# Kernel tuning notes

Hardware: AMD Instinct MI355X
Metric: run time of the kernel (lower is better)

The kernel has to match this reference:

```python
import jax, jax.numpy as jnp
import numpy as np

B, H, S, DK = 2, 16, 2048, 64


def setup_inputs() -> dict:
    key = jax.random.key(0)
    kq, kk, kv = jax.random.split(key, 3)
    query = jax.random.normal(kq, (B, H, S, DK), dtype=jnp.float32)
    k = jax.random.normal(kk, (B, H, S, DK), dtype=jnp.float32)
    value = jax.random.normal(kv, (B, H, S, DK), dtype=jnp.float32)
    # causal padding-style mask: 1 = keep, 0 = masked (set to -inf pre-softmax)
    mask = jnp.tril(jnp.ones((S, S), dtype=jnp.int32))[None, None, :, :]
    return {"query": query, "key": k, "value": value, "d_k": DK, "mask": mask}


def reference(query, key, value, d_k, mask):
    # scores: [B, H, Sq, Sk]
    scores = jnp.einsum("bhqd,bhkd->bhqk", query, key)
    scores = scores / jnp.sqrt(jnp.asarray(d_k, dtype=scores.dtype))
    scores = jnp.where(mask == 0, -jnp.inf, scores)
    att = jax.nn.softmax(scores, axis=-1)
    # dropout is identity in eval mode (deterministic reference)
    out = jnp.einsum("bhqk,bhkd->bhqd", att, value)
    return out
```

## Files before the change

kernel.cpp:

```cpp
#include <hip/hip_runtime.h>
#include <cstdint>

#define B_ 2
#define H_ 16
#define S_ 2048
#define DK_ 64
#define BH_ (B_*H_)
#define NQT 32
#define BN 128

typedef __attribute__((ext_vector_type(8))) short short8;
typedef __attribute__((ext_vector_type(4))) float floatx4;

__device__ inline unsigned short f2bf(float f) {
  union { float f; unsigned u; } v; v.f = f;
  unsigned u = v.u;
  unsigned r = u + 0x7fffu + ((u >> 16) & 1u);
  return (unsigned short)(r >> 16);
}

__global__ __launch_bounds__(256) void conv_kv(const float* __restrict__ K,
                                               const float* __restrict__ V,
                                               unsigned short* __restrict__ Kb,
                                               unsigned short* __restrict__ Vb) {
  __shared__ __align__(16) unsigned short t[64 * 80];
  const int bh = blockIdx.y, s0 = blockIdx.x * 64;
  const int row = threadIdx.x >> 2, cp = threadIdx.x & 3;

  {
    const float* src = K + ((size_t)(bh * S_ + s0 + row)) * DK_ + cp * 16;
    unsigned short* dst = Kb + ((size_t)(bh * S_ + s0 + row)) * DK_ + cp * 16;
    #pragma unroll
    for (int h = 0; h < 2; ++h) {
      float4 a = *(const float4*)(src + h * 8);
      float4 b = *(const float4*)(src + h * 8 + 4);
      uint4 st;
      st.x = (unsigned)f2bf(a.x) | ((unsigned)f2bf(a.y) << 16);
      st.y = (unsigned)f2bf(a.z) | ((unsigned)f2bf(a.w) << 16);
      st.z = (unsigned)f2bf(b.x) | ((unsigned)f2bf(b.y) << 16);
      st.w = (unsigned)f2bf(b.z) | ((unsigned)f2bf(b.w) << 16);
      *(uint4*)(dst + h * 8) = st;
    }
  }
  {
    const float* src = V + ((size_t)(bh * S_ + s0 + row)) * DK_ + cp * 16;
    #pragma unroll
    for (int j4 = 0; j4 < 4; ++j4) {
      float4 a = *(const float4*)(src + j4 * 4);
      int c = cp * 16 + j4 * 4;
      t[(c + 0) * 80 + row] = f2bf(a.x);
      t[(c + 1) * 80 + row] = f2bf(a.y);
      t[(c + 2) * 80 + row] = f2bf(a.z);
      t[(c + 3) * 80 + row] = f2bf(a.w);
    }
    __syncthreads();
    unsigned short* dst = Vb + ((size_t)(bh * DK_ + row)) * S_ + s0 + cp * 16;
    *(uint4*)(dst)     = *(const uint4*)&t[row * 80 + cp * 16];
    *(uint4*)(dst + 8) = *(const uint4*)&t[row * 80 + cp * 16 + 8];
  }
}

__global__ __launch_bounds__(256, 2)
void fa_kernel(const float* __restrict__ Q, const unsigned short* __restrict__ Kb,
               const unsigned short* __restrict__ Vb, float* __restrict__ Out) {
  __shared__ __align__(16) unsigned short Kt[2][8192];
  __shared__ __align__(16) unsigned short Vt[2][8192];
  __shared__ __align__(16) unsigned short Pt[8192];

  const int tid  = threadIdx.x;
  const int wave = tid >> 6;
  const int lane = tid & 63;
  const int quad = lane >> 4;
  const int l16  = lane & 15;
  const int bh   = blockIdx.y;
  const int qa   = blockIdx.x;
  const int qb   = NQT - 1 - qa;

  const float SCL = 0.125f * 1.44269504088896340736f;

  short8 aqA[2], aqB[2];
  {
    const float* qgA = Q + ((size_t)bh * S_ + qa * 64 + wave * 16 + l16) * DK_;
    const float* qgB = Q + ((size_t)bh * S_ + qb * 64 + wave * 16 + l16) * DK_;
    #pragma unroll
    for (int ks = 0; ks < 2; ++ks) {
      float4 x = *(const float4*)(qgA + ks * 32 + quad * 8);
      float4 y = *(const float4*)(qgA + ks * 32 + quad * 8 + 4);
      short8 t;
      t[0]=(short)f2bf(x.x*SCL); t[1]=(short)f2bf(x.y*SCL); t[2]=(short)f2bf(x.z*SCL); t[3]=(short)f2bf(x.w*SCL);
      t[4]=(short)f2bf(y.x*SCL); t[5]=(short)f2bf(y.y*SCL); t[6]=(short)f2bf(y.z*SCL); t[7]=(short)f2bf(y.w*SCL);
      aqA[ks] = t;
      x = *(const float4*)(qgB + ks * 32 + quad * 8);
      y = *(const float4*)(qgB + ks * 32 + quad * 8 + 4);
      t[0]=(short)f2bf(x.x*SCL); t[1]=(short)f2bf(x.y*SCL); t[2]=(short)f2bf(x.z*SCL); t[3]=(short)f2bf(x.w*SCL);
      t[4]=(short)f2bf(y.x*SCL); t[5]=(short)f2bf(y.y*SCL); t[6]=(short)f2bf(y.z*SCL); t[7]=(short)f2bf(y.w*SCL);
      aqB[ks] = t;
    }
  }

  floatx4 OA[4], OB[4];
  float lA[4], lB[4];
  #pragma unroll
  for (int nt = 0; nt < 4; ++nt) { OA[nt] = (floatx4){0,0,0,0}; OB[nt] = (floatx4){0,0,0,0}; }
  #pragma unroll
  for (int r = 0; r < 4; ++r) { lA[r] = 0.f; lB[r] = 0.f; }

  auto stage = [&](int buf, int kv) {
    #pragma unroll
    for (int rd = 0; rd < 4; ++rd) {
      int cid = rd * 256 + wave * 64 + lane;
      {
        int row = cid >> 3, p = cid & 7, c = p ^ (row & 7);
        const unsigned short* g = Kb + (((size_t)bh * S_ + kv * BN + row) << 6) + (c << 3);
        __builtin_amdgcn_global_load_lds(
            (const __attribute__((address_space(1))) void*)g,
            (__attribute__((address_space(3))) void*)&Kt[buf][(rd * 4 + wave) * 512], 16, 0, 0);
      }
      {
        int row = cid >> 4, p = cid & 15, c = p ^ (row & 15);
        const unsigned short* g = Vb + (((size_t)bh * DK_ + row) << 11) + kv * BN + (c << 3);
        __builtin_amdgcn_global_load_lds(
            (const __attribute__((address_space(1))) void*)g,
            (__attribute__((address_space(3))) void*)&Vt[buf][(rd * 4 + wave) * 512], 16, 0, 0);
      }
    }
  };

  auto compute = [&](const short8* aq, floatx4* Ot, float* lsum,
                     int qt, int kv, int cur, bool domask) {
    float sc[8][4];
    #pragma unroll
    for (int nt = 0; nt < 8; ++nt) {
      floatx4 acc = (floatx4){0.f, 0.f, 0.f, 0.f};
      #pragma unroll
      for (int ks = 0; ks < 2; ++ks) {
        int row = nt * 16 + l16;
        int p = (ks * 4 + quad) ^ (row & 7);
        const short8 bk = *(const short8*)&Kt[cur][row * 64 + p * 8];
        acc = __builtin_amdgcn_mfma_f32_16x16x32_bf16(aq[ks], bk, acc, 0, 0, 0);
      }
      #pragma unroll
      for (int r = 0; r < 4; ++r) sc[nt][r] = acc[r];
    }
    if (domask) {
      #pragma unroll
      for (int nt = 0; nt < 8; ++nt) {
        int col = kv * BN + nt * 16 + l16;
        #pragma unroll
        for (int r = 0; r < 4; ++r) {
          int rowg = qt * 64 + wave * 16 + quad * 4 + r;
          if (col > rowg) sc[nt][r] = -INFINITY;
        }
      }
    }
    #pragma unroll
    for (int nt = 0; nt < 8; ++nt)
      #pragma unroll
      for (int r = 0; r < 4; ++r) {
        float e = __builtin_amdgcn_exp2f(sc[nt][r]);
        lsum[r] += e;
        sc[nt][r] = e;
      }
    __builtin_amdgcn_s_waitcnt(0xC07F);
    __builtin_amdgcn_wave_barrier();
    #pragma unroll
    for (int nt = 0; nt < 8; ++nt) {
      int c = nt * 2 + (l16 >> 3);
      #pragma unroll
      for (int r = 0; r < 4; ++r) {
        int row16 = quad * 4 + r;
        int p = c ^ row16;
        Pt[wave * 2048 + row16 * 128 + p * 8 + (l16 & 7)] = f2bf(sc[nt][r]);
      }
    }
    __builtin_amdgcn_wave_barrier();
    __builtin_amdgcn_s_waitcnt(0xC07F);
    #pragma unroll
    for (int ks = 0; ks < 4; ++ks) {
      int pr = (ks * 4 + quad) ^ l16;
      const short8 ap = *(const short8*)&Pt[wave * 2048 + l16 * 128 + pr * 8];
      #pragma unroll
      for (int nt = 0; nt < 4; ++nt) {
        int row = nt * 16 + l16;
        int p = (ks * 4 + quad) ^ (row & 15);
        const short8 bv = *(const short8*)&Vt[cur][row * 128 + p * 8];
        Ot[nt] = __builtin_amdgcn_mfma_f32_16x16x32_bf16(ap, bv, Ot[nt], 0, 0, 0);
      }
    }
  };

  stage(0, 0);
  __syncthreads();
  const int nkvB = (qb + 2) >> 1;
  const int nkvA = (qa + 2) >> 1;
  for (int kv = 0; kv < nkvB; ++kv) {
    int cur = kv & 1;
    if (kv + 1 < nkvB) stage(cur ^ 1, kv + 1);
    compute(aqB, OB, lB, qb, kv, cur, kv == nkvB - 1);
    if (kv < nkvA) compute(aqA, OA, lA, qa, kv, cur, kv == nkvA - 1);
    __syncthreads();
  }

  #pragma unroll
  for (int r = 0; r < 4; ++r) {
    lB[r] += __shfl_xor(lB[r], 1); lB[r] += __shfl_xor(lB[r], 2);
    lB[r] += __shfl_xor(lB[r], 4); lB[r] += __shfl_xor(lB[r], 8);
    lA[r] += __shfl_xor(lA[r], 1); lA[r] += __shfl_xor(lA[r], 2);
    lA[r] += __shfl_xor(lA[r], 4); lA[r] += __shfl_xor(lA[r], 8);
  }
  {
    float* Og = Out + ((size_t)bh * S_ + qb * 64 + wave * 16) * DK_;
    #pragma unroll
    for (int r = 0; r < 4; ++r) {
      float inv = 1.0f / lB[r];
      #pragma unroll
      for (int nt = 0; nt < 4; ++nt)
        Og[(quad * 4 + r) * DK_ + nt * 16 + l16] = OB[nt][r] * inv;
    }
    Og = Out + ((size_t)bh * S_ + qa * 64 + wave * 16) * DK_;
    #pragma unroll
    for (int r = 0; r < 4; ++r) {
      float inv = 1.0f / lA[r];
      #pragma unroll
      for (int nt = 0; nt < 4; ++nt)
        Og[(quad * 4 + r) * DK_ + nt * 16 + l16] = OA[nt][r] * inv;
    }
  }
}

extern "C" void kernel_launch(void* const* d_in, const int* in_sizes, int n_in,
                              void* d_out, int out_size, void* d_ws, size_t ws_size,
                              hipStream_t stream) {
  const float* Q = (const float*)d_in[0];
  const float* K = (const float*)d_in[1];
  const float* V = (const float*)d_in[2];
  float* Out = (float*)d_out;
  unsigned short* Kb = (unsigned short*)d_ws;
  unsigned short* Vb = Kb + (size_t)BH_ * S_ * DK_;
  conv_kv<<<dim3(S_ / 64, BH_), 256, 0, stream>>>(K, V, Kb, Vb);
  fa_kernel<<<dim3(NQT / 2, BH_), 256, 0, stream>>>(Q, Kb, Vb, Out);
}
```

Before: 146.7 us.

## Compute transposed S=K·Qᵀ, keep P in registers, split KV across waves

Swaps the score MFMA operands so each lane holds scores along the key dimension, then packs exp values straight to bf16 in registers and feeds them to a 16x16x16 MFMA as the B operand. This removes the per-wave LDS round trip for P. V is stored pre-permuted in the conversion kernel to match the new register layout. Waves are split into a 2x2 grid over query halves and KV halves, and the partial O and row sums are reduced through LDS at the end. The 1D grid is also remapped so that blocks with the same qa are adjacent in launch order. This adds an end-of-kernel reduction and uses round-half-up bf16 packing, which rounds slightly differently from the old round-to-nearest-even.

```diff
diff --git a/kernel.cpp b/kernel.cpp
--- a/kernel.cpp
+++ b/kernel.cpp
@@ -7,9 +7,9 @@
 #define DK_ 64
 #define BH_ (B_*H_)
 #define NQT 32
-#define BN 128
 
 typedef __attribute__((ext_vector_type(8))) short short8;
+typedef __attribute__((ext_vector_type(4))) short short4v;
 typedef __attribute__((ext_vector_type(4))) float floatx4;
 
 __device__ inline unsigned short f2bf(float f) {
@@ -17,6 +17,21 @@
   unsigned u = v.u;
   unsigned r = u + 0x7fffu + ((u >> 16) & 1u);
   return (unsigned short)(r >> 16);
+}
+
+__device__ inline floatx4 mfma16(short4v a, short4v b, floatx4 c) {
+#if __has_builtin(__builtin_amdgcn_mfma_f32_16x16x16bf16_1k)
+  return __builtin_amdgcn_mfma_f32_16x16x16bf16_1k(a, b, c, 0, 0, 0);
+#else
+  asm("v_mfma_f32_16x16x16_bf16 %0, %1, %2, %0" : "+v"(c) : "v"(a), "v"(b));
+  return c;
+#endif
+}
+
+__device__ inline short4v u2s4(unsigned a, unsigned b) {
+  union { unsigned u[2]; short4v s; } v;
+  v.u[0] = a; v.u[1] = b;
+  return v.s;
 }
 
 __global__ __launch_bounds__(256) void conv_kv(const float* __restrict__ K,
@@ -54,9 +69,13 @@
       t[(c + 3) * 80 + row] = f2bf(a.w);
     }
     __syncthreads();
-    unsigned short* dst = Vb + ((size_t)(bh * DK_ + row)) * S_ + s0 + cp * 16;
-    *(uint4*)(dst)     = *(const uint4*)&t[row * 80 + cp * 16];
-    *(uint4*)(dst + 8) = *(const uint4*)&t[row * 80 + cp * 16 + 8];
+    const int base128 = s0 & ~127;
+    const int t2 = 2 * ((s0 >> 6) & 1) + (cp >> 1);
+    const int h  = cp & 1;
+    unsigned short* dst = Vb + ((size_t)(bh * DK_ + row)) * S_ + base128 + t2 * 32 + h * 4;
+    #pragma unroll
+    for (int q = 0; q < 4; ++q)
+      *(uint2*)(dst + q * 8) = *(const uint2*)&t[row * 80 + cp * 16 + q * 4];
   }
 }
 
@@ -65,60 +84,62 @@
                const unsigned short* __restrict__ Vb, float* __restrict__ Out) {
   __shared__ __align__(16) unsigned short Kt[2][8192];
   __shared__ __align__(16) unsigned short Vt[2][8192];
-  __shared__ __align__(16) unsigned short Pt[8192];
 
   const int tid  = threadIdx.x;
   const int wave = tid >> 6;
   const int lane = tid & 63;
   const int quad = lane >> 4;
   const int l16  = lane & 15;
-  const int bh   = blockIdx.y;
-  const int qa   = blockIdx.x;
-  const int qb   = NQT - 1 - qa;
+  const int wq   = wave & 1;
+  const int ws   = wave >> 1;
+
+  const int id = blockIdx.x;
+  const int bh = (id & 7) | (((id >> 3) & 3) << 3);
+  const int qa = id >> 5;
+  const int qb = NQT - 1 - qa;
 
   const float SCL = 0.125f * 1.44269504088896340736f;
 
-  short8 aqA[2], aqB[2];
-  {
-    const float* qgA = Q + ((size_t)bh * S_ + qa * 64 + wave * 16 + l16) * DK_;
-    const float* qgB = Q + ((size_t)bh * S_ + qb * 64 + wave * 16 + l16) * DK_;
-    #pragma unroll
-    for (int ks = 0; ks < 2; ++ks) {
-      float4 x = *(const float4*)(qgA + ks * 32 + quad * 8);
-      float4 y = *(const float4*)(qgA + ks * 32 + quad * 8 + 4);
-      short8 t;
-      t[0]=(short)f2bf(x.x*SCL); t[1]=(short)f2bf(x.y*SCL); t[2]=(short)f2bf(x.z*SCL); t[3]=(short)f2bf(x.w*SCL);
-      t[4]=(short)f2bf(y.x*SCL); t[5]=(short)f2bf(y.y*SCL); t[6]=(short)f2bf(y.z*SCL); t[7]=(short)f2bf(y.w*SCL);
-      aqA[ks] = t;
-      x = *(const float4*)(qgB + ks * 32 + quad * 8);
-      y = *(const float4*)(qgB + ks * 32 + quad * 8 + 4);
-      t[0]=(short)f2bf(x.x*SCL); t[1]=(short)f2bf(x.y*SCL); t[2]=(short)f2bf(x.z*SCL); t[3]=(short)f2bf(x.w*SCL);
-      t[4]=(short)f2bf(y.x*SCL); t[5]=(short)f2bf(y.y*SCL); t[6]=(short)f2bf(y.z*SCL); t[7]=(short)f2bf(y.w*SCL);
-      aqB[ks] = t;
-    }
-  }
-
-  floatx4 OA[4], OB[4];
-  float lA[4], lB[4];
+  short8 qfB[4], qfA[4];
+  auto loadQ = [&](int qt, short8* qf) {
+    #pragma unroll
+    for (int nq = 0; nq < 2; ++nq) {
+      const float* p = Q + ((size_t)bh * S_ + qt * 64 + wq * 32 + nq * 16 + l16) * DK_ + quad * 8;
+      #pragma unroll
+      for (int ks = 0; ks < 2; ++ks) {
+        float4 x = *(const float4*)(p + ks * 32);
+        float4 y = *(const float4*)(p + ks * 32 + 4);
+        short8 t;
+        t[0]=(short)f2bf(x.x*SCL); t[1]=(short)f2bf(x.y*SCL); t[2]=(short)f2bf(x.z*SCL); t[3]=(short)f2bf(x.w*SCL);
+        t[4]=(short)f2bf(y.x*SCL); t[5]=(short)f2bf(y.y*SCL); t[6]=(short)f2bf(y.z*SCL); t[7]=(short)f2bf(y.w*SCL);
+        qf[nq * 2 + ks] = t;
+      }
+    }
+  };
+  loadQ(qb, qfB);
+  loadQ(qa, qfA);
+
+  floatx4 OtB[4][2], OtA[4][2];
+  float lB_[2] = {0.f, 0.f}, lA_[2] = {0.f, 0.f};
   #pragma unroll
-  for (int nt = 0; nt < 4; ++nt) { OA[nt] = (floatx4){0,0,0,0}; OB[nt] = (floatx4){0,0,0,0}; }
-  #pragma unroll
-  for (int r = 0; r < 4; ++r) { lA[r] = 0.f; lB[r] = 0.f; }
+  for (int d = 0; d < 4; ++d)
+    #pragma unroll
+    for (int nq = 0; nq < 2; ++nq) { OtB[d][nq] = (floatx4){0,0,0,0}; OtA[d][nq] = (floatx4){0,0,0,0}; }
 
   auto stage = [&](int buf, int kv) {
     #pragma unroll
     for (int rd = 0; rd < 4; ++rd) {
-      int cid = rd * 256 + wave * 64 + lane;
+      const int cid = rd * 256 + wave * 64 + lane;
       {
         int row = cid >> 3, p = cid & 7, c = p ^ (row & 7);
-        const unsigned short* g = Kb + (((size_t)bh * S_ + kv * BN + row) << 6) + (c << 3);
+        const unsigned short* g = Kb + (((size_t)bh * S_ + kv * 128 + row) << 6) + (c << 3);
         __builtin_amdgcn_global_load_lds(
             (const __attribute__((address_space(1))) void*)g,
             (__attribute__((address_space(3))) void*)&Kt[buf][(rd * 4 + wave) * 512], 16, 0, 0);
       }
       {
         int row = cid >> 4, p = cid & 15, c = p ^ (row & 15);
-        const unsigned short* g = Vb + (((size_t)bh * DK_ + row) << 11) + kv * BN + (c << 3);
+        const unsigned short* g = Vb + (((size_t)bh * DK_ + row) << 11) + kv * 128 + (c << 3);
         __builtin_amdgcn_global_load_lds(
             (const __attribute__((address_space(1))) void*)g,
             (__attribute__((address_space(3))) void*)&Vt[buf][(rd * 4 + wave) * 512], 16, 0, 0);
@@ -126,65 +147,57 @@
     }
   };
 
-  auto compute = [&](const short8* aq, floatx4* Ot, float* lsum,
-                     int qt, int kv, int cur, bool domask) {
-    float sc[8][4];
-    #pragma unroll
-    for (int nt = 0; nt < 8; ++nt) {
-      floatx4 acc = (floatx4){0.f, 0.f, 0.f, 0.f};
+  auto computeT = [&](const short8* qf, floatx4 (*Ot)[2], float* ls,
+                      int qt, int kv, int cur, bool domask) {
+    unsigned pk[4][2][2];
+    #pragma unroll
+    for (int nt = 0; nt < 4; ++nt) {
+      const int row = ws * 64 + nt * 16 + l16;
+      floatx4 s0 = (floatx4){0,0,0,0}, s1 = (floatx4){0,0,0,0};
       #pragma unroll
       for (int ks = 0; ks < 2; ++ks) {
-        int row = nt * 16 + l16;
-        int p = (ks * 4 + quad) ^ (row & 7);
-        const short8 bk = *(const short8*)&Kt[cur][row * 64 + p * 8];
-        acc = __builtin_amdgcn_mfma_f32_16x16x32_bf16(aq[ks], bk, acc, 0, 0, 0);
-      }
-      #pragma unroll
-      for (int r = 0; r < 4; ++r) sc[nt][r] = acc[r];
-    }
-    if (domask) {
-      #pragma unroll
-      for (int nt = 0; nt < 8; ++nt) {
-        int col = kv * BN + nt * 16 + l16;
+        const int p = (ks * 4 + quad) ^ (row & 7);
+        const short8 ak = *(const short8*)&Kt[cur][row * 64 + p * 8];
+        s0 = __builtin_amdgcn_mfma_f32_16x16x32_bf16(ak, qf[ks],     s0, 0, 0, 0);
+        s1 = __builtin_amdgcn_mfma_f32_16x16x32_bf16(ak, qf[2 + ks], s1, 0, 0, 0);
+      }
+      if (domask) {
+        const int sb  = kv * 128 + ws * 64 + nt * 16 + quad * 4;
+        const int q0r = qt * 64 + wq * 32 + l16;
         #pragma unroll
         for (int r = 0; r < 4; ++r) {
-          int rowg = qt * 64 + wave * 16 + quad * 4 + r;
-          if (col > rowg) sc[nt][r] = -INFINITY;
-        }
-      }
-    }
-    #pragma unroll
-    for (int nt = 0; nt < 8; ++nt)
-      #pragma unroll
-      for (int r = 0; r < 4; ++r) {
-        float e = __builtin_amdgcn_exp2f(sc[nt][r]);
-        lsum[r] += e;
-        sc[nt][r] = e;
-      }
-    __builtin_amdgcn_s_waitcnt(0xC07F);
-    __builtin_amdgcn_wave_barrier();
-    #pragma unroll
-    for (int nt = 0; nt < 8; ++nt) {
-      int c = nt * 2 + (l16 >> 3);
-      #pragma unroll
-      for (int r = 0; r < 4; ++r) {
-        int row16 = quad * 4 + r;
-        int p = c ^ row16;
-        Pt[wave * 2048 + row16 * 128 + p * 8 + (l16 & 7)] = f2bf(sc[nt][r]);
-      }
-    }
-    __builtin_amdgcn_wave_barrier();
-    __builtin_amdgcn_s_waitcnt(0xC07F);
-    #pragma unroll
-    for (int ks = 0; ks < 4; ++ks) {
-      int pr = (ks * 4 + quad) ^ l16;
-      const short8 ap = *(const short8*)&Pt[wave * 2048 + l16 * 128 + pr * 8];
-      #pragma unroll
-      for (int nt = 0; nt < 4; ++nt) {
-        int row = nt * 16 + l16;
-        int p = (ks * 4 + quad) ^ (row & 15);
-        const short8 bv = *(const short8*)&Vt[cur][row * 128 + p * 8];
-        Ot[nt] = __builtin_amdgcn_mfma_f32_16x16x32_bf16(ap, bv, Ot[nt], 0, 0, 0);
+          if (sb + r > q0r)      s0[r] = -INFINITY;
+          if (sb + r > q0r + 16) s1[r] = -INFINITY;
+        }
+      }
+      #pragma unroll
+      for (int nq = 0; nq < 2; ++nq) {
+        const floatx4 sv = nq ? s1 : s0;
+        float e0 = __builtin_amdgcn_exp2f(sv[0]);
+        float e1 = __builtin_amdgcn_exp2f(sv[1]);
+        float e2 = __builtin_amdgcn_exp2f(sv[2]);
+        float e3 = __builtin_amdgcn_exp2f(sv[3]);
+        ls[nq] += (e0 + e1) + (e2 + e3);
+        pk[nt][nq][0] = __builtin_amdgcn_perm(__float_as_uint(e1) + 0x8000u,
+                                              __float_as_uint(e0) + 0x8000u, 0x07060302u);
+        pk[nt][nq][1] = __builtin_amdgcn_perm(__float_as_uint(e3) + 0x8000u,
+                                              __float_as_uint(e2) + 0x8000u, 0x07060302u);
+      }
+    }
+    #pragma unroll
+    for (int dblk = 0; dblk < 4; ++dblk) {
+      const int row = dblk * 16 + l16;
+      #pragma unroll
+      for (int tt = 0; tt < 2; ++tt) {
+        const int p = ((ws * 2 + tt) * 4 + quad) ^ l16;
+        const short8 v8 = *(const short8*)&Vt[cur][row * 128 + p * 8];
+        const short4v vlo = __builtin_shufflevector(v8, v8, 0, 1, 2, 3);
+        const short4v vhi = __builtin_shufflevector(v8, v8, 4, 5, 6, 7);
+        #pragma unroll
+        for (int nq = 0; nq < 2; ++nq) {
+          Ot[dblk][nq] = mfma16(vlo, u2s4(pk[2*tt  ][nq][0], pk[2*tt  ][nq][1]), Ot[dblk][nq]);
+          Ot[dblk][nq] = mfma16(vhi, u2s4(pk[2*tt+1][nq][0], pk[2*tt+1][nq][1]), Ot[dblk][nq]);
+        }
       }
     }
   };
@@ -194,36 +207,57 @@
   const int nkvB = (qb + 2) >> 1;
   const int nkvA = (qa + 2) >> 1;
   for (int kv = 0; kv < nkvB; ++kv) {
-    int cur = kv & 1;
+    const int cur = kv & 1;
     if (kv + 1 < nkvB) stage(cur ^ 1, kv + 1);
-    compute(aqB, OB, lB, qb, kv, cur, kv == nkvB - 1);
-    if (kv < nkvA) compute(aqA, OA, lA, qa, kv, cur, kv == nkvA - 1);
+    computeT(qfB, OtB, lB_, qb, kv, cur, kv == nkvB - 1);
+    if (kv < nkvA) computeT(qfA, OtA, lA_, qa, kv, cur, kv == nkvA - 1);
     __syncthreads();
   }
 
   #pragma unroll
-  for (int r = 0; r < 4; ++r) {
-    lB[r] += __shfl_xor(lB[r], 1); lB[r] += __shfl_xor(lB[r], 2);
-    lB[r] += __shfl_xor(lB[r], 4); lB[r] += __shfl_xor(lB[r], 8);
-    lA[r] += __shfl_xor(lA[r], 1); lA[r] += __shfl_xor(lA[r], 2);
-    lA[r] += __shfl_xor(lA[r], 4); lA[r] += __shfl_xor(lA[r], 8);
-  }
-  {
-    float* Og = Out + ((size_t)bh * S_ + qb * 64 + wave * 16) * DK_;
-    #pragma unroll
-    for (int r = 0; r < 4; ++r) {
-      float inv = 1.0f / lB[r];
-      #pragma unroll
-      for (int nt = 0; nt < 4; ++nt)
-        Og[(quad * 4 + r) * DK_ + nt * 16 + l16] = OB[nt][r] * inv;
-    }
-    Og = Out + ((size_t)bh * S_ + qa * 64 + wave * 16) * DK_;
-    #pragma unroll
-    for (int r = 0; r < 4; ++r) {
-      float inv = 1.0f / lA[r];
-      #pragma unroll
-      for (int nt = 0; nt < 4; ++nt)
-        Og[(quad * 4 + r) * DK_ + nt * 16 + l16] = OA[nt][r] * inv;
+  for (int nq = 0; nq < 2; ++nq) {
+    lB_[nq] += __shfl_xor(lB_[nq], 16); lB_[nq] += __shfl_xor(lB_[nq], 32);
+    lA_[nq] += __shfl_xor(lA_[nq], 16); lA_[nq] += __shfl_xor(lA_[nq], 32);
+  }
+  float* OP = (float*)&Kt[0][0];
+  float* LP = (float*)&Vt[0][0];
+  if (ws == 1) {
+    #pragma unroll
+    for (int tile = 0; tile < 2; ++tile) {
+      floatx4 (*Ot)[2] = tile ? OtA : OtB;
+      const float* ls  = tile ? lA_ : lB_;
+      #pragma unroll
+      for (int nq = 0; nq < 2; ++nq) {
+        const int rowi = ((wq * 2 + tile) * 2 + nq) * 16 + l16;
+        #pragma unroll
+        for (int dblk = 0; dblk < 4; ++dblk) {
+          const int c2 = (dblk * 4 + quad) ^ (l16 & 12);
+          *(floatx4*)&OP[rowi * 64 + c2 * 4] = Ot[dblk][nq];
+        }
+        if (quad == 0) LP[rowi] = ls[nq];
+      }
+    }
+  }
+  __syncthreads();
+  if (ws == 0) {
+    #pragma unroll
+    for (int tile = 0; tile < 2; ++tile) {
+      floatx4 (*Ot)[2] = tile ? OtA : OtB;
+      const float* ls  = tile ? lA_ : lB_;
+      const int qt     = tile ? qa : qb;
+      #pragma unroll
+      for (int nq = 0; nq < 2; ++nq) {
+        const int rowi = ((wq * 2 + tile) * 2 + nq) * 16 + l16;
+        const float inv = 1.0f / (ls[nq] + LP[rowi]);
+        float* og = Out + ((size_t)bh * S_ + qt * 64 + wq * 32 + nq * 16 + l16) * DK_;
+        #pragma unroll
+        for (int dblk = 0; dblk < 4; ++dblk) {
+          const int c2 = (dblk * 4 + quad) ^ (l16 & 12);
+          floatx4 tot = Ot[dblk][nq] + *(const floatx4*)&OP[rowi * 64 + c2 * 4];
+          tot *= inv;
+          *(floatx4*)(og + dblk * 16 + quad * 4) = tot;
+        }
+      }
     }
   }
 }
@@ -238,5 +272,5 @@
   unsigned short* Kb = (unsigned short*)d_ws;
   unsigned short* Vb = Kb + (size_t)BH_ * S_ * DK_;
   conv_kv<<<dim3(S_ / 64, BH_), 256, 0, stream>>>(K, V, Kb, Vb);
-  fa_kernel<<<dim3(NQT / 2, BH_), 256, 0, stream>>>(Q, Kb, Vb, Out);
-}
+  fa_kernel<<<dim3(512), 256, 0, stream>>>(Q, Kb, Vb, Out);
+}
```

New measurement: 139.7 us. 1.05x faster.
